# Kernel tuning notes

Measured on AMD Instinct MI355X. Metric: run time of the kernel, lower is better.

## Reference

```python
import jax, jax.numpy as jnp
import numpy as np

I4_CLIP = 7.0
NUM_HEADS = 16
NUM_KV_HEADS = 4
HEAD_DIM = 64
ROPE_BASE = 10000.0


def fake_quant_i4(w):
    # per-row int4 symmetric fake quantization with straight-through estimator
    row_max = jnp.maximum(jnp.max(jnp.abs(w), axis=-1, keepdims=True), 1e-8)
    scale = row_max / I4_CLIP
    w_deq = jnp.clip(jnp.round(w / scale), -I4_CLIP, I4_CLIP) * scale
    return w + jax.lax.stop_gradient(w_deq - w)


def rms_norm(x):
    eps = jnp.asarray(jnp.finfo(x.dtype).eps, x.dtype)
    return x * jax.lax.rsqrt(jnp.mean(x * x, axis=-1, keepdims=True) + eps)


def rope_cos_sin(seqlen, dtype):
    inv_freq = 1.0 / (ROPE_BASE ** (jnp.arange(0, HEAD_DIM, 2, dtype=jnp.float32) / HEAD_DIM))
    freqs = jnp.outer(jnp.arange(seqlen, dtype=jnp.float32), inv_freq)  # [S, hd/2]
    return jnp.cos(freqs).astype(dtype), jnp.sin(freqs).astype(dtype)


def apply_rotary(x, cos, sin):
    # x: [B, H, S, hd]; cos/sin: [S, hd/2] broadcast over B, H
    half = x.shape[-1] // 2
    x1, x2 = x[..., :half], x[..., half:]
    return jnp.concatenate((x1 * cos + x2 * sin, -x1 * sin + x2 * cos), axis=-1)


def setup_inputs() -> dict:
    key = jax.random.key(0)
    ks = jax.random.split(key, 6)
    dim = NUM_HEADS * HEAD_DIM
    kv_dim = NUM_KV_HEADS * HEAD_DIM
    return {
        "x": jax.random.normal(ks[0], (2, 2048, dim), jnp.float32),
        "w_q": jax.random.normal(ks[1], (dim, dim), jnp.float32) * 0.02,
        "w_k": jax.random.normal(ks[2], (kv_dim, dim), jnp.float32) * 0.02,
        "w_v": jax.random.normal(ks[3], (kv_dim, dim), jnp.float32) * 0.02,
        "w_proj": jax.random.normal(ks[4], (dim, dim), jnp.float32) * 0.02,
        "q_gain": jnp.ones((NUM_HEADS,), jnp.float32),
    }


def reference(x, w_q, w_k, w_v, w_proj, q_gain):
    bsz, seqlen, dim = x.shape
    rep = NUM_HEADS // NUM_KV_HEADS

    wq, wk, wv, wp = (fake_quant_i4(w) for w in (w_q, w_k, w_v, w_proj))

    # projections: F.linear(x, W) = x @ W.T -> [B, S, out]; split heads -> [B, H, S, hd]
    q = (x @ wq.T).reshape(bsz, seqlen, NUM_HEADS, HEAD_DIM).transpose(0, 2, 1, 3)
    k = (x @ wk.T).reshape(bsz, seqlen, NUM_KV_HEADS, HEAD_DIM).transpose(0, 2, 1, 3)
    v = (x @ wv.T).reshape(bsz, seqlen, NUM_KV_HEADS, HEAD_DIM).transpose(0, 2, 1, 3)

    q, k = rms_norm(q), rms_norm(k)
    cos, sin = rope_cos_sin(seqlen, q.dtype)
    q = apply_rotary(q, cos, sin)
    k = apply_rotary(k, cos, sin)
    q = q * q_gain.astype(q.dtype)[None, :, None, None]

    # GQA: expand kv heads
    k = jnp.repeat(k, rep, axis=1)
    v = jnp.repeat(v, rep, axis=1)

    # causal SDPA
    scale = 1.0 / np.sqrt(HEAD_DIM)
    scores = jnp.einsum("bhqd,bhkd->bhqk", q, k) * scale
    causal = jnp.tril(jnp.ones((seqlen, seqlen), dtype=bool))
    scores = jnp.where(causal, scores, jnp.asarray(-jnp.inf, scores.dtype))
    attn = jax.nn.softmax(scores, axis=-1)
    y = jnp.einsum("bhqk,bhkd->bhqd", attn, v)

    y = y.transpose(0, 2, 1, 3).reshape(bsz, seqlen, dim)
    return y @ wp.T
```

## Files before the change

kernel.cpp:

```cpp
#include <hip/hip_runtime.h>


typedef __bf16 bf16x8 __attribute__((ext_vector_type(8)));
typedef __bf16 bf16x4 __attribute__((ext_vector_type(4)));
typedef float  f32x4  __attribute__((ext_vector_type(4)));

__device__ __forceinline__ unsigned short f2bf(float f) {
  __bf16 h = (__bf16)f;
  return __builtin_bit_cast(unsigned short, h);
}

__global__ void prep(const float* __restrict__ wq, const float* __restrict__ wk,
                     const float* __restrict__ wv, const float* __restrict__ wp,
                     const float* __restrict__ x,
                     unsigned short* __restrict__ wqkv,
                     unsigned short* __restrict__ wpb,
                     unsigned short* __restrict__ x_bf) {
  int bid = blockIdx.x;
  int t = threadIdx.x;
  if (bid >= 2560) {
    int i = ((bid - 2560) * 256 + t) * 4;
    float4 f = *(const float4*)(x + i);
    ushort4 o;
    o.x = f2bf(f.x); o.y = f2bf(f.y); o.z = f2bf(f.z); o.w = f2bf(f.w);
    *(ushort4*)(x_bf + i) = o;
    return;
  }
  int row = bid;
  const float* s;
  unsigned short* d;
  if (row < 1024)      { s = wq + (size_t)row * 1024;          d = wqkv + (size_t)row * 1024; }
  else if (row < 1280) { s = wk + (size_t)(row - 1024) * 1024; d = wqkv + (size_t)row * 1024; }
  else if (row < 1536) { s = wv + (size_t)(row - 1280) * 1024; d = wqkv + (size_t)row * 1024; }
  else                 { s = wp + (size_t)(row - 1536) * 1024; d = wpb + (size_t)(row - 1536) * 1024; }
  float4 v = *(const float4*)(s + t * 4);
  float mx = fmaxf(fmaxf(fabsf(v.x), fabsf(v.y)), fmaxf(fabsf(v.z), fabsf(v.w)));
#pragma unroll
  for (int m = 1; m < 64; m <<= 1) mx = fmaxf(mx, __shfl_xor(mx, m));
  __shared__ float smx[4];
  if ((t & 63) == 0) smx[t >> 6] = mx;
  __syncthreads();
  mx = fmaxf(fmaxf(smx[0], smx[1]), fmaxf(smx[2], smx[3]));
  mx = fmaxf(mx, 1e-8f);
  float scale = mx / 7.0f;
  float q0 = fminf(fmaxf(rintf(v.x / scale), -7.0f), 7.0f);
  float q1 = fminf(fmaxf(rintf(v.y / scale), -7.0f), 7.0f);
  float q2 = fminf(fmaxf(rintf(v.z / scale), -7.0f), 7.0f);
  float q3 = fminf(fmaxf(rintf(v.w / scale), -7.0f), 7.0f);
  ushort4 o;
  o.x = f2bf(q0 * scale); o.y = f2bf(q1 * scale);
  o.z = f2bf(q2 * scale); o.w = f2bf(q3 * scale);
  *(ushort4*)(d + t * 4) = o;
}

#define GLDS(g, l)                                                            \
  __builtin_amdgcn_global_load_lds((const __attribute__((address_space(1))) void*)(g), \
                                   (__attribute__((address_space(3))) void*)(l), 16, 0, 0)

__global__ __launch_bounds__(512, 4) void gemm_bt(
    const unsigned short* __restrict__ A, const unsigned short* __restrict__ Bw,
    float* __restrict__ C, int N, int K, int nbn) {
  int bm = blockIdx.x / nbn, bn = blockIdx.x % nbn;
  int tid = threadIdx.x, w = tid >> 6, lane = tid & 63;
  int l15 = lane & 15, lh = lane >> 4;
  __shared__ __align__(16) unsigned short ldsA[2][128 * 64];
  __shared__ __align__(16) unsigned short ldsB[2][128 * 64];
  int wr = w >> 1, wc = w & 1;
  f32x4 zero = {0.f, 0.f, 0.f, 0.f};
  f32x4 acc[2][4];
#pragma unroll
  for (int i = 0; i < 2; i++)
#pragma unroll
    for (int j = 0; j < 4; j++) acc[i][j] = zero;

  int srow = lane >> 3, schunk = (lane & 7) ^ (lane >> 3);
  const unsigned short* gA0 = A  + (size_t)(bm * 128 + srow) * K + schunk * 8;
  const unsigned short* gB0 = Bw + (size_t)(bn * 128 + srow) * K + schunk * 8;

  int nk = K >> 6;
#pragma unroll
  for (int it = 0; it < 2; it++) {
    int seg = w * 2 + it;
    GLDS(gA0 + (size_t)(seg * 8) * K, (unsigned short*)ldsA[0] + seg * 512);
    GLDS(gB0 + (size_t)(seg * 8) * K, (unsigned short*)ldsB[0] + seg * 512);
  }
  __syncthreads();
  int cur = 0;
  for (int kt = 0; kt < nk; kt++) {
    if (kt + 1 < nk) {
      int k0 = (kt + 1) * 64;
#pragma unroll
      for (int it = 0; it < 2; it++) {
        int seg = w * 2 + it;
        GLDS(gA0 + (size_t)(seg * 8) * K + k0, (unsigned short*)ldsA[cur ^ 1] + seg * 512);
        GLDS(gB0 + (size_t)(seg * 8) * K + k0, (unsigned short*)ldsB[cur ^ 1] + seg * 512);
      }
    }
    const unsigned short* cA = ldsA[cur];
    const unsigned short* cB = ldsB[cur];
#pragma unroll
    for (int ks = 0; ks < 2; ks++) {
      bf16x8 af[2], bfr[4];
#pragma unroll
      for (int fm = 0; fm < 2; fm++) {
        int row = wr * 32 + fm * 16 + l15;
        int slot = (ks * 4 + lh) ^ (row & 7);
        af[fm] = *(const bf16x8*)(cA + row * 64 + slot * 8);
      }
#pragma unroll
      for (int fn = 0; fn < 4; fn++) {
        int row = wc * 64 + fn * 16 + l15;
        int slot = (ks * 4 + lh) ^ (row & 7);
        bfr[fn] = *(const bf16x8*)(cB + row * 64 + slot * 8);
      }
#pragma unroll
      for (int fm = 0; fm < 2; fm++)
#pragma unroll
        for (int fn = 0; fn < 4; fn++)
          acc[fm][fn] = __builtin_amdgcn_mfma_f32_16x16x32_bf16(af[fm], bfr[fn], acc[fm][fn], 0, 0, 0);
    }
    __syncthreads();
    cur ^= 1;
  }
#pragma unroll
  for (int fm = 0; fm < 2; fm++) {
    int r0 = bm * 128 + wr * 32 + fm * 16 + lh * 4;
#pragma unroll
    for (int fn = 0; fn < 4; fn++) {
      int c = bn * 128 + wc * 64 + fn * 16 + l15;
#pragma unroll
      for (int reg = 0; reg < 4; reg++)
        C[(size_t)(r0 + reg) * N + c] = acc[fm][fn][reg];
    }
  }
}

__global__ __launch_bounds__(512, 4) void gemm_qkv(
    const unsigned short* __restrict__ A, const unsigned short* __restrict__ Bw,
    const float* __restrict__ gainp,
    unsigned short* __restrict__ qb, unsigned short* __restrict__ kbp,
    unsigned short* __restrict__ vbp) {
  const int K = 1024;
  int bm = blockIdx.x / 12, bn = blockIdx.x % 12;
  int tid = threadIdx.x, w = tid >> 6, lane = tid & 63;
  int l15 = lane & 15, lh = lane >> 4;
  __shared__ __align__(16) unsigned short ldsA[2][128 * 64];
  __shared__ __align__(16) unsigned short ldsB[2][128 * 64];
  int wr = w >> 1, wc = w & 1;
  f32x4 zero = {0.f, 0.f, 0.f, 0.f};
  f32x4 acc[2][4];
#pragma unroll
  for (int i = 0; i < 2; i++)
#pragma unroll
    for (int j = 0; j < 4; j++) acc[i][j] = zero;

  int srow = lane >> 3, schunk = (lane & 7) ^ (lane >> 3);
  const unsigned short* gA0 = A  + (size_t)(bm * 128 + srow) * K + schunk * 8;
  const unsigned short* gB0 = Bw + (size_t)(bn * 128 + srow) * K + schunk * 8;

#pragma unroll
  for (int it = 0; it < 2; it++) {
    int seg = w * 2 + it;
    GLDS(gA0 + (size_t)(seg * 8) * K, (unsigned short*)ldsA[0] + seg * 512);
    GLDS(gB0 + (size_t)(seg * 8) * K, (unsigned short*)ldsB[0] + seg * 512);
  }
  __syncthreads();
  int cur = 0;
  for (int kt = 0; kt < 16; kt++) {
    if (kt + 1 < 16) {
      int k0 = (kt + 1) * 64;
#pragma unroll
      for (int it = 0; it < 2; it++) {
        int seg = w * 2 + it;
        GLDS(gA0 + (size_t)(seg * 8) * K + k0, (unsigned short*)ldsA[cur ^ 1] + seg * 512);
        GLDS(gB0 + (size_t)(seg * 8) * K + k0, (unsigned short*)ldsB[cur ^ 1] + seg * 512);
      }
    }
    const unsigned short* cA = ldsA[cur];
    const unsigned short* cB = ldsB[cur];
#pragma unroll
    for (int ks = 0; ks < 2; ks++) {
      bf16x8 af[2], bfr[4];
#pragma unroll
      for (int fm = 0; fm < 2; fm++) {
        int row = wr * 32 + fm * 16 + l15;
        int slot = (ks * 4 + lh) ^ (row & 7);
        af[fm] = *(const bf16x8*)(cA + row * 64 + slot * 8);
      }
#pragma unroll
      for (int fn = 0; fn < 4; fn++) {
        int row = wc * 64 + fn * 16 + l15;
        int slot = (ks * 4 + lh) ^ (row & 7);
        bfr[fn] = *(const bf16x8*)(cB + row * 64 + slot * 8);
      }
#pragma unroll
      for (int fm = 0; fm < 2; fm++)
#pragma unroll
        for (int fn = 0; fn < 4; fn++)
          acc[fm][fn] = __builtin_amdgcn_mfma_f32_16x16x32_bf16(af[fm], bfr[fn], acc[fm][fn], 0, 0, 0);
    }
    __syncthreads();
    cur ^= 1;
  }

  int hid = bn * 2 + wc;
  int rbase = bm * 128 + wr * 32;
  if (hid >= 20) {
    int vh = hid - 20;
#pragma unroll
    for (int fm = 0; fm < 2; fm++)
#pragma unroll
      for (int reg = 0; reg < 4; reg++) {
        int r = rbase + fm * 16 + lh * 4 + reg;
        int b = r >> 11, s = r & 2047;
        unsigned short* dst = vbp + (((size_t)(b * 4 + vh) * 2048 + s) << 6);
#pragma unroll
        for (int fn = 0; fn < 4; fn++)
          dst[fn * 16 + l15] = f2bf(acc[fm][fn][reg]);
      }
  } else {
    bool isq = hid < 16;
    float gn = isq ? gainp[hid] : 1.0f;
    float invf0 = __expf(-0.28782313662425572f * (float)l15);
    float invf1 = __expf(-0.28782313662425572f * (float)(l15 + 16));
#pragma unroll
    for (int fm = 0; fm < 2; fm++)
#pragma unroll
      for (int reg = 0; reg < 4; reg++) {
        float y0 = acc[fm][0][reg], y1 = acc[fm][1][reg];
        float y2 = acc[fm][2][reg], y3 = acc[fm][3][reg];
        float ss = y0 * y0 + y1 * y1 + y2 * y2 + y3 * y3;
        ss += __shfl_xor(ss, 1); ss += __shfl_xor(ss, 2);
        ss += __shfl_xor(ss, 4); ss += __shfl_xor(ss, 8);
        float rn = rsqrtf(ss * 0.015625f + 1.1920929e-7f);
        y0 *= rn; y1 *= rn; y2 *= rn; y3 *= rn;
        int r = rbase + fm * 16 + lh * 4 + reg;
        int b = r >> 11, s = r & 2047;
        float c0, s0n, c1, s1n;
        __sincosf((float)s * invf0, &s0n, &c0);
        __sincosf((float)s * invf1, &s1n, &c1);
        float o0 = (y0 * c0 + y2 * s0n) * gn;
        float o1 = (y1 * c1 + y3 * s1n) * gn;
        float o2 = (y2 * c0 - y0 * s0n) * gn;
        float o3 = (y3 * c1 - y1 * s1n) * gn;
        unsigned short* dst = isq
          ? qb  + (((size_t)(b * 16 + hid) * 2048 + s) << 6)
          : kbp + (((size_t)(b * 4 + (hid - 16)) * 2048 + s) << 6);
        dst[l15]      = f2bf(o0);
        dst[l15 + 16] = f2bf(o1);
        dst[l15 + 32] = f2bf(o2);
        dst[l15 + 48] = f2bf(o3);
      }
  }
}

__global__ void v_transpose(const unsigned short* __restrict__ vbp,
                            unsigned short* __restrict__ vt) {
  int bid = blockIdx.x;
  int st = bid & 31, bk = bid >> 5;
  __shared__ unsigned short tile[64][72];
  int t = threadIdx.x;
  int sl = t >> 2, d0 = (t & 3) * 16;
  const unsigned short* src = vbp + (((size_t)bk * 2048 + st * 64 + sl) << 6) + d0;
  *(ushort4*)&tile[sl][d0]      = *(const ushort4*)(src);
  *(ushort4*)&tile[sl][d0 + 4]  = *(const ushort4*)(src + 4);
  *(ushort4*)&tile[sl][d0 + 8]  = *(const ushort4*)(src + 8);
  *(ushort4*)&tile[sl][d0 + 12] = *(const ushort4*)(src + 12);
  __syncthreads();
  int d = t >> 2, p0 = (t & 3) * 16;
  unsigned short* dst = vt + ((size_t)bk * 64 + d) * 2048 + st * 64 + p0;
#pragma unroll
  for (int jo = 0; jo < 16; jo += 4) {
    ushort4 a;
#pragma unroll
    for (int j = 0; j < 4; j++) {
      int p = p0 + jo + j;
      int c = ((p & 3) << 4) | (p >> 2);
      ((unsigned short*)&a)[j] = tile[c][d];
    }
    *(ushort4*)(dst + jo) = a;
  }
}

#define PSTR 72

template<bool MASK>
__device__ __forceinline__ void attn_tile(
    int kv0, int q0, int l15, int lh, float M2,
    const unsigned short* ldsK, const unsigned short* ldsV, unsigned short* pw,
    const bf16x8 (&qf)[2][2], float (&lsum)[2][4], f32x4 (&o)[2][4]) {
  const float K2 = 0.18033688011112042f;
  f32x4 zero = {0.f, 0.f, 0.f, 0.f};
  f32x4 sc[2][4];
#pragma unroll
  for (int fm = 0; fm < 2; fm++)
#pragma unroll
    for (int fn = 0; fn < 4; fn++) sc[fm][fn] = zero;
#pragma unroll
  for (int ks = 0; ks < 2; ks++) {
    bf16x8 kf[4];
#pragma unroll
    for (int fn = 0; fn < 4; fn++) {
      int row = fn * 16 + l15;
      int slot = (ks * 4 + lh) ^ (row & 7);
      kf[fn] = *(const bf16x8*)(ldsK + row * 64 + slot * 8);
    }
#pragma unroll
    for (int fm = 0; fm < 2; fm++)
#pragma unroll
      for (int fn = 0; fn < 4; fn++)
        sc[fm][fn] = __builtin_amdgcn_mfma_f32_16x16x32_bf16(qf[fm][ks], kf[fn], sc[fm][fn], 0, 0, 0);
  }
  bf16x8 vf[2][4];
#pragma unroll
  for (int ks2 = 0; ks2 < 2; ks2++)
#pragma unroll
    for (int fn = 0; fn < 4; fn++) {
      int row = fn * 16 + l15;
      int slot = (ks2 * 4 + lh) ^ (row & 7);
      vf[ks2][fn] = *(const bf16x8*)(ldsV + row * 64 + slot * 8);
    }
#pragma unroll
  for (int fm = 0; fm < 2; fm++)
#pragma unroll
    for (int r = 0; r < 4; r++) {
      bf16x4 pk;
      float ls = 0.f;
#pragma unroll
      for (int fn = 0; fn < 4; fn++) {
        float s = __builtin_fmaf(sc[fm][fn][r], K2, -M2);
        if (MASK) {
          int col = kv0 + fn * 16 + l15;
          int row = q0 + fm * 16 + lh * 4 + r;
          if (col > row) s = -1e30f;
        }
        float p = __builtin_amdgcn_exp2f(s);
        ls += p;
        pk[fn] = (__bf16)p;
      }
      *(bf16x4*)(pw + (fm * 16 + lh * 4 + r) * PSTR + l15 * 4) = pk;
      lsum[fm][r] += ls;
    }
  asm volatile("s_waitcnt lgkmcnt(0)" ::: "memory");
  __builtin_amdgcn_sched_barrier(0);
#pragma unroll
  for (int ks2 = 0; ks2 < 2; ks2++) {
    bf16x8 pf[2];
#pragma unroll
    for (int fm = 0; fm < 2; fm++)
      pf[fm] = *(const bf16x8*)(pw + (fm * 16 + l15) * PSTR + ks2 * 32 + lh * 8);
#pragma unroll
    for (int fm = 0; fm < 2; fm++)
#pragma unroll
      for (int fn = 0; fn < 4; fn++)
        o[fm][fn] = __builtin_amdgcn_mfma_f32_16x16x32_bf16(pf[fm], vf[ks2][fn], o[fm][fn], 0, 0, 0);
  }
}

__global__ __launch_bounds__(256, 3) void attn_fwd(
    const unsigned short* __restrict__ qbuf, const unsigned short* __restrict__ kb,
    const unsigned short* __restrict__ vtb, const float* __restrict__ gain,
    unsigned short* __restrict__ ob, unsigned short* __restrict__ pO,
    float* __restrict__ pL) {
  int bid = blockIdx.x;
  int cid = bid >> 5;
  int bh = bid & 31;
  int b = bh >> 4, h = bh & 15;
  int qb = 0, cum = 0;
  for (int q = 0; q < 16; q++) {
    int ncq = (2 * q + 5) >> 2;
    if (cid < cum + ncq) { qb = q; break; }
    cum += ncq;
  }
  int nt = 2 * qb + 2;
  int nc = (2 * qb + 5) >> 2;
  int ch = cid - cum;
  int base = nt / nc, rem = nt % nc;
  int t0 = ch * base + (ch < rem ? ch : rem);
  int t1 = t0 + base + (ch < rem ? 1 : 0);
  bool direct = (nc == 1);

  int tid = threadIdx.x;
  int w = tid >> 6, lane = tid & 63;
  int l15 = lane & 15, lh = lane >> 4;
  int q0 = qb * 128 + w * 32;
  int kvh = h >> 2;
  const unsigned short* Q  = qbuf + (size_t)(b * 16 + h) * (2048 * 64);
  const unsigned short* Kg = kb   + (size_t)(b * 4 + kvh) * (2048 * 64);
  const unsigned short* Vg = vtb  + (size_t)(b * 4 + kvh) * (64 * 2048);

  __shared__ __align__(16) unsigned short ldsK[2][64 * 64];
  __shared__ __align__(16) unsigned short ldsV[2][64 * 64];
  __shared__ __align__(16) unsigned short plds[4][32 * PSTR];
  unsigned short* pw = plds[w];

  float gn = gain[h];
  float M2 = __builtin_fmaf(fabsf(gn), 1.46f, 0.02f);

  bf16x8 qf[2][2];
#pragma unroll
  for (int fm = 0; fm < 2; fm++)
#pragma unroll
    for (int ks = 0; ks < 2; ks++)
      qf[fm][ks] = *(const bf16x8*)(Q + (q0 + fm * 16 + l15) * 64 + ks * 32 + lh * 8);

  f32x4 zero = {0.f, 0.f, 0.f, 0.f};
  f32x4 o[2][4];
  float lsum[2][4];
#pragma unroll
  for (int fm = 0; fm < 2; fm++)
#pragma unroll
    for (int r = 0; r < 4; r++) { lsum[fm][r] = 0.f; o[fm][r] = zero; }

  int srow = lane >> 3;
  int schunk = (lane & 7) ^ (lane >> 3);
  int full = q0 >> 6;

#pragma unroll
  for (int it = 0; it < 2; it++) {
    int seg = w * 2 + it;
    GLDS(Kg + (size_t)(t0 * 64 + seg * 8 + srow) * 64 + schunk * 8,
         (unsigned short*)ldsK[0] + seg * 512);
    GLDS(Vg + (size_t)(seg * 8 + srow) * 2048 + t0 * 64 + schunk * 8,
         (unsigned short*)ldsV[0] + seg * 512);
  }
  __syncthreads();
  int cur = 0;
  for (int t = t0; t < t1; t++) {
    int kv0 = t * 64;
    if (t + 1 < t1) {
      int kn = kv0 + 64;
#pragma unroll
      for (int it = 0; it < 2; it++) {
        int seg = w * 2 + it;
        GLDS(Kg + (size_t)(kn + seg * 8 + srow) * 64 + schunk * 8,
             (unsigned short*)ldsK[cur ^ 1] + seg * 512);
        GLDS(Vg + (size_t)(seg * 8 + srow) * 2048 + kn + schunk * 8,
             (unsigned short*)ldsV[cur ^ 1] + seg * 512);
      }
    }
    if (t < full)
      attn_tile<false>(kv0, q0, l15, lh, M2, ldsK[cur], ldsV[cur], pw, qf, lsum, o);
    else if (kv0 <= q0 + 31)
      attn_tile<true>(kv0, q0, l15, lh, M2, ldsK[cur], ldsV[cur], pw, qf, lsum, o);
    __syncthreads();
    cur ^= 1;
  }

  if (direct) {
#pragma unroll
    for (int fm = 0; fm < 2; fm++)
#pragma unroll
      for (int r = 0; r < 4; r++) {
        float l = lsum[fm][r];
        l += __shfl_xor(l, 1); l += __shfl_xor(l, 2);
        l += __shfl_xor(l, 4); l += __shfl_xor(l, 8);
        float inv = 1.0f / l;
        int row = q0 + fm * 16 + lh * 4 + r;
#pragma unroll
        for (int fn = 0; fn < 4; fn++)
          ob[(size_t)(b * 2048 + row) * 1024 + h * 64 + fn * 16 + l15] =
              f2bf(o[fm][fn][r] * inv);
      }
  } else {
    int slot = bh * 70 + (cid - 2);
    unsigned short* po = pO + ((size_t)slot << 13);
    float* pl = pL + slot * 128;
#pragma unroll
    for (int fm = 0; fm < 2; fm++)
#pragma unroll
      for (int r = 0; r < 4; r++) {
        float l = lsum[fm][r];
        l += __shfl_xor(l, 1); l += __shfl_xor(l, 2);
        l += __shfl_xor(l, 4); l += __shfl_xor(l, 8);
        int row = w * 32 + fm * 16 + lh * 4 + r;
        if (l15 == 0) pl[row] = l;
        bf16x4 pv;
#pragma unroll
        for (int fn = 0; fn < 4; fn++) pv[fn] = (__bf16)o[fm][fn][r];
        *(bf16x4*)(po + row * 64 + l15 * 4) = pv;
      }
  }
}

__global__ __launch_bounds__(128) void attn_finalize(
    const unsigned short* __restrict__ pO, const float* __restrict__ pL,
    unsigned short* __restrict__ ob) {
  int bid = blockIdx.x;
  int qb = 2 + bid % 14;
  int bh = bid / 14;
  int b = bh >> 4, h = bh & 15;
  int cum = 0;
  for (int q = 0; q < 16; q++) {
    if (q == qb) break;
    cum += (2 * q + 5) >> 2;
  }
  int nc = (2 * qb + 5) >> 2;
  int s0 = bh * 70 + (cum - 2);

  int row = threadIdx.x;
  float acc[64];
#pragma unroll
  for (int j = 0; j < 64; j++) acc[j] = 0.f;
  float l = 0.f;
  for (int c = 0; c < nc; c++) {
    const unsigned short* po = pO + (((size_t)(s0 + c)) << 13) + row * 64;
    l += pL[(s0 + c) * 128 + row];
#pragma unroll
    for (int j = 0; j < 8; j++) {
      uint4 u = *(const uint4*)(po + j * 8);
      const unsigned short* us = (const unsigned short*)&u;
#pragma unroll
      for (int e = 0; e < 8; e++) {
        unsigned int bits = (unsigned int)us[e] << 16;
        acc[j * 8 + e] += __builtin_bit_cast(float, bits);
      }
    }
  }
  float inv = 1.0f / l;
  unsigned short* dst = ob + (size_t)(b * 2048 + qb * 128 + row) * 1024 + h * 64;
  unsigned short outv[64];
#pragma unroll
  for (int c = 0; c < 64; c++) {
    int pos = (c & 15) * 4 + (c >> 4);
    outv[c] = f2bf(acc[pos] * inv);
  }
#pragma unroll
  for (int j = 0; j < 8; j++)
    *(uint4*)(dst + j * 8) = *(const uint4*)(outv + j * 8);
}

extern "C" void kernel_launch(void* const* d_in, const int* in_sizes, int n_in,
                              void* d_out, int out_size, void* d_ws, size_t ws_size,
                              hipStream_t stream) {
  const float* x    = (const float*)d_in[0];
  const float* w_q  = (const float*)d_in[1];
  const float* w_k  = (const float*)d_in[2];
  const float* w_v  = (const float*)d_in[3];
  const float* w_p  = (const float*)d_in[4];
  const float* gain = (const float*)d_in[5];
  float* out = (float*)d_out;

  char* ws = (char*)d_ws;
  unsigned short* x_bf  = (unsigned short*)ws;
  unsigned short* wqkv  = (unsigned short*)(ws + (8u << 20));
  unsigned short* wp    = (unsigned short*)(ws + (11u << 20));
  unsigned short* qbuf  = (unsigned short*)(ws + (13u << 20));
  unsigned short* kbuf  = (unsigned short*)(ws + (21u << 20));
  unsigned short* vbuf  = (unsigned short*)(ws + (23u << 20));
  unsigned short* vtbuf = (unsigned short*)(ws + (25u << 20));
  unsigned short* aout  = (unsigned short*)(ws + (27u << 20));
  unsigned short* pO    = (unsigned short*)(ws + (35u << 20));
  float*          pL    = (float*)(ws + (73u << 20));

  prep<<<6656, 256, 0, stream>>>(w_q, w_k, w_v, w_p, x, wqkv, wp, x_bf);
  gemm_qkv<<<32 * 12, 512, 0, stream>>>(x_bf, wqkv, gain, qbuf, kbuf, vbuf);
  v_transpose<<<256, 256, 0, stream>>>(vbuf, vtbuf);
  attn_fwd<<<2304, 256, 0, stream>>>(qbuf, kbuf, vtbuf, gain, aout, pO, pL);
  attn_finalize<<<448, 128, 0, stream>>>(pO, pL, aout);
  gemm_bt<<<32 * 8, 512, 0, stream>>>(aout, wp, out, 1024, 1024, 8);
}
```

Measured before the change: 102.1 us.

## Switch attention to 32x32x16 MFMA with register-resident P via permlane swap

New measurement: 100.0 us. 1.02x faster.

```diff
diff --git a/kernel.cpp b/kernel.cpp
--- a/kernel.cpp
+++ b/kernel.cpp
@@ -2,8 +2,9 @@
 
 
 typedef __bf16 bf16x8 __attribute__((ext_vector_type(8)));
-typedef __bf16 bf16x4 __attribute__((ext_vector_type(4)));
 typedef float  f32x4  __attribute__((ext_vector_type(4)));
+typedef float  f32x16 __attribute__((ext_vector_type(16)));
+typedef int    i32x4  __attribute__((ext_vector_type(4)));
 
 __device__ __forceinline__ unsigned short f2bf(float f) {
   __bf16 h = (__bf16)f;
@@ -273,87 +274,72 @@
   for (int jo = 0; jo < 16; jo += 4) {
     ushort4 a;
 #pragma unroll
-    for (int j = 0; j < 4; j++) {
-      int p = p0 + jo + j;
-      int c = ((p & 3) << 4) | (p >> 2);
-      ((unsigned short*)&a)[j] = tile[c][d];
-    }
+    for (int j = 0; j < 4; j++)
+      ((unsigned short*)&a)[j] = tile[p0 + jo + j][d];
     *(ushort4*)(dst + jo) = a;
   }
 }
-
-#define PSTR 72
 
 template<bool MASK>
 __device__ __forceinline__ void attn_tile(
-    int kv0, int q0, int l15, int lh, float M2,
-    const unsigned short* ldsK, const unsigned short* ldsV, unsigned short* pw,
-    const bf16x8 (&qf)[2][2], float (&lsum)[2][4], f32x4 (&o)[2][4]) {
+    int kv0, int q0, int l31, int hi, float M2,
+    const unsigned short* ldsK, const unsigned short* ldsV,
+    const bf16x8 (&qf)[4], float& lsum, f32x16 (&o)[2]) {
   const float K2 = 0.18033688011112042f;
-  f32x4 zero = {0.f, 0.f, 0.f, 0.f};
-  f32x4 sc[2][4];
-#pragma unroll
-  for (int fm = 0; fm < 2; fm++)
-#pragma unroll
-    for (int fn = 0; fn < 4; fn++) sc[fm][fn] = zero;
-#pragma unroll
-  for (int ks = 0; ks < 2; ks++) {
-    bf16x8 kf[4];
-#pragma unroll
-    for (int fn = 0; fn < 4; fn++) {
-      int row = fn * 16 + l15;
-      int slot = (ks * 4 + lh) ^ (row & 7);
-      kf[fn] = *(const bf16x8*)(ldsK + row * 64 + slot * 8);
-    }
-#pragma unroll
-    for (int fm = 0; fm < 2; fm++)
-#pragma unroll
-      for (int fn = 0; fn < 4; fn++)
-        sc[fm][fn] = __builtin_amdgcn_mfma_f32_16x16x32_bf16(qf[fm][ks], kf[fn], sc[fm][fn], 0, 0, 0);
-  }
-  bf16x8 vf[2][4];
-#pragma unroll
-  for (int ks2 = 0; ks2 < 2; ks2++)
-#pragma unroll
-    for (int fn = 0; fn < 4; fn++) {
-      int row = fn * 16 + l15;
-      int slot = (ks2 * 4 + lh) ^ (row & 7);
-      vf[ks2][fn] = *(const bf16x8*)(ldsV + row * 64 + slot * 8);
-    }
-#pragma unroll
-  for (int fm = 0; fm < 2; fm++)
-#pragma unroll
-    for (int r = 0; r < 4; r++) {
-      bf16x4 pk;
-      float ls = 0.f;
-#pragma unroll
-      for (int fn = 0; fn < 4; fn++) {
-        float s = __builtin_fmaf(sc[fm][fn][r], K2, -M2);
+  f32x16 sc[2];
+#pragma unroll
+  for (int i = 0; i < 16; i++) { sc[0][i] = 0.f; sc[1][i] = 0.f; }
+#pragma unroll
+  for (int ks = 0; ks < 4; ks++) {
+    int slot0 = (2 * ks + hi) ^ (l31 & 7);
+    bf16x8 kf0 = *(const bf16x8*)(ldsK + l31 * 64 + slot0 * 8);
+    int row1 = 32 + l31;
+    int slot1 = (2 * ks + hi) ^ (row1 & 7);
+    bf16x8 kf1 = *(const bf16x8*)(ldsK + row1 * 64 + slot1 * 8);
+    sc[0] = __builtin_amdgcn_mfma_f32_32x32x16_bf16(kf0, qf[ks], sc[0], 0, 0, 0);
+    sc[1] = __builtin_amdgcn_mfma_f32_32x32x16_bf16(kf1, qf[ks], sc[1], 0, 0, 0);
+  }
+  unsigned int Wp[2][4][2];
+  float ls = 0.f;
+  int rowq = q0 + l31;
+#pragma unroll
+  for (int fn = 0; fn < 2; fn++)
+#pragma unroll
+    for (int g = 0; g < 4; g++) {
+      float p4[4];
+#pragma unroll
+      for (int m = 0; m < 4; m++) {
+        int r = 4 * g + m;
+        float s = __builtin_fmaf(sc[fn][r], K2, -M2);
         if (MASK) {
-          int col = kv0 + fn * 16 + l15;
-          int row = q0 + fm * 16 + lh * 4 + r;
-          if (col > row) s = -1e30f;
+          int col = kv0 + fn * 32 + m + 8 * g + 4 * hi;
+          if (col > rowq) s = -1e30f;
         }
         float p = __builtin_amdgcn_exp2f(s);
         ls += p;
-        pk[fn] = (__bf16)p;
-      }
-      *(bf16x4*)(pw + (fm * 16 + lh * 4 + r) * PSTR + l15 * 4) = pk;
-      lsum[fm][r] += ls;
-    }
-  asm volatile("s_waitcnt lgkmcnt(0)" ::: "memory");
-  __builtin_amdgcn_sched_barrier(0);
-#pragma unroll
-  for (int ks2 = 0; ks2 < 2; ks2++) {
-    bf16x8 pf[2];
-#pragma unroll
-    for (int fm = 0; fm < 2; fm++)
-      pf[fm] = *(const bf16x8*)(pw + (fm * 16 + l15) * PSTR + ks2 * 32 + lh * 8);
-#pragma unroll
-    for (int fm = 0; fm < 2; fm++)
-#pragma unroll
-      for (int fn = 0; fn < 4; fn++)
-        o[fm][fn] = __builtin_amdgcn_mfma_f32_16x16x32_bf16(pf[fm], vf[ks2][fn], o[fm][fn], 0, 0, 0);
+        p4[m] = p;
+      }
+      asm("v_cvt_pk_bf16_f32 %0, %1, %2" : "=v"(Wp[fn][g][0]) : "v"(p4[0]), "v"(p4[1]));
+      asm("v_cvt_pk_bf16_f32 %0, %1, %2" : "=v"(Wp[fn][g][1]) : "v"(p4[2]), "v"(p4[3]));
+    }
+  lsum += ls;
+#pragma unroll
+  for (int ksg = 0; ksg < 4; ksg++) {
+    int fn = ksg >> 1, e = ksg & 1;
+    unsigned int u0 = Wp[fn][2 * e][0], u1 = Wp[fn][2 * e + 1][0];
+    unsigned int u2 = Wp[fn][2 * e][1], u3 = Wp[fn][2 * e + 1][1];
+    asm("v_permlane32_swap_b32 %0, %1" : "+v"(u0), "+v"(u1));
+    asm("v_permlane32_swap_b32 %0, %1" : "+v"(u2), "+v"(u3));
+    i32x4 pw;
+    pw[0] = (int)u0; pw[1] = (int)u2; pw[2] = (int)u1; pw[3] = (int)u3;
+    bf16x8 pf = __builtin_bit_cast(bf16x8, pw);
+    int slot0 = (2 * ksg + hi) ^ (l31 & 7);
+    bf16x8 v0 = *(const bf16x8*)(ldsV + l31 * 64 + slot0 * 8);
+    int row1 = 32 + l31;
+    int slot1 = (2 * ksg + hi) ^ (row1 & 7);
+    bf16x8 v1 = *(const bf16x8*)(ldsV + row1 * 64 + slot1 * 8);
+    o[0] = __builtin_amdgcn_mfma_f32_32x32x16_bf16(pf, v0, o[0], 0, 0, 0);
+    o[1] = __builtin_amdgcn_mfma_f32_32x32x16_bf16(pf, v1, o[1], 0, 0, 0);
   }
 }
 
@@ -382,7 +368,7 @@
 
   int tid = threadIdx.x;
   int w = tid >> 6, lane = tid & 63;
-  int l15 = lane & 15, lh = lane >> 4;
+  int l31 = lane & 31, hi = lane >> 5;
   int q0 = qb * 128 + w * 32;
   int kvh = h >> 2;
   const unsigned short* Q  = qbuf + (size_t)(b * 16 + h) * (2048 * 64);
@@ -391,26 +377,19 @@
 
   __shared__ __align__(16) unsigned short ldsK[2][64 * 64];
   __shared__ __align__(16) unsigned short ldsV[2][64 * 64];
-  __shared__ __align__(16) unsigned short plds[4][32 * PSTR];
-  unsigned short* pw = plds[w];
 
   float gn = gain[h];
   float M2 = __builtin_fmaf(fabsf(gn), 1.46f, 0.02f);
 
-  bf16x8 qf[2][2];
-#pragma unroll
-  for (int fm = 0; fm < 2; fm++)
-#pragma unroll
-    for (int ks = 0; ks < 2; ks++)
-      qf[fm][ks] = *(const bf16x8*)(Q + (q0 + fm * 16 + l15) * 64 + ks * 32 + lh * 8);
-
-  f32x4 zero = {0.f, 0.f, 0.f, 0.f};
-  f32x4 o[2][4];
-  float lsum[2][4];
-#pragma unroll
-  for (int fm = 0; fm < 2; fm++)
-#pragma unroll
-    for (int r = 0; r < 4; r++) { lsum[fm][r] = 0.f; o[fm][r] = zero; }
+  bf16x8 qf[4];
+#pragma unroll
+  for (int ks = 0; ks < 4; ks++)
+    qf[ks] = *(const bf16x8*)(Q + (size_t)(q0 + l31) * 64 + ks * 16 + hi * 8);
+
+  f32x16 o[2];
+#pragma unroll
+  for (int i = 0; i < 16; i++) { o[0][i] = 0.f; o[1][i] = 0.f; }
+  float lsum = 0.f;
 
   int srow = lane >> 3;
   int schunk = (lane & 7) ^ (lane >> 3);
@@ -440,46 +419,36 @@
       }
     }
     if (t < full)
-      attn_tile<false>(kv0, q0, l15, lh, M2, ldsK[cur], ldsV[cur], pw, qf, lsum, o);
+      attn_tile<false>(kv0, q0, l31, hi, M2, ldsK[cur], ldsV[cur], qf, lsum, o);
     else if (kv0 <= q0 + 31)
-      attn_tile<true>(kv0, q0, l15, lh, M2, ldsK[cur], ldsV[cur], pw, qf, lsum, o);
+      attn_tile<true>(kv0, q0, l31, hi, M2, ldsK[cur], ldsV[cur], qf, lsum, o);
     __syncthreads();
     cur ^= 1;
   }
 
+  float lred = lsum + __shfl_xor(lsum, 32);
   if (direct) {
-#pragma unroll
-    for (int fm = 0; fm < 2; fm++)
-#pragma unroll
-      for (int r = 0; r < 4; r++) {
-        float l = lsum[fm][r];
-        l += __shfl_xor(l, 1); l += __shfl_xor(l, 2);
-        l += __shfl_xor(l, 4); l += __shfl_xor(l, 8);
-        float inv = 1.0f / l;
-        int row = q0 + fm * 16 + lh * 4 + r;
-#pragma unroll
-        for (int fn = 0; fn < 4; fn++)
-          ob[(size_t)(b * 2048 + row) * 1024 + h * 64 + fn * 16 + l15] =
-              f2bf(o[fm][fn][r] * inv);
-      }
+    float linv = 1.0f / lred;
+#pragma unroll
+    for (int r = 0; r < 16; r++) {
+      int qr = (r & 3) + 8 * (r >> 2) + 4 * hi;
+      float iv = __shfl(linv, qr);
+      size_t rb = (size_t)(b * 2048 + q0 + qr) * 1024 + h * 64;
+      ob[rb + l31]      = f2bf(o[0][r] * iv);
+      ob[rb + 32 + l31] = f2bf(o[1][r] * iv);
+    }
   } else {
     int slot = bh * 70 + (cid - 2);
     unsigned short* po = pO + ((size_t)slot << 13);
     float* pl = pL + slot * 128;
-#pragma unroll
-    for (int fm = 0; fm < 2; fm++)
-#pragma unroll
-      for (int r = 0; r < 4; r++) {
-        float l = lsum[fm][r];
-        l += __shfl_xor(l, 1); l += __shfl_xor(l, 2);
-        l += __shfl_xor(l, 4); l += __shfl_xor(l, 8);
-        int row = w * 32 + fm * 16 + lh * 4 + r;
-        if (l15 == 0) pl[row] = l;
-        bf16x4 pv;
-#pragma unroll
-        for (int fn = 0; fn < 4; fn++) pv[fn] = (__bf16)o[fm][fn][r];
-        *(bf16x4*)(po + row * 64 + l15 * 4) = pv;
-      }
+    if (lane < 32) pl[w * 32 + l31] = lred;
+#pragma unroll
+    for (int r = 0; r < 16; r++) {
+      int qr = (r & 3) + 8 * (r >> 2) + 4 * hi;
+      int row = w * 32 + qr;
+      po[row * 64 + l31]      = f2bf(o[0][r]);
+      po[row * 64 + 32 + l31] = f2bf(o[1][r]);
+    }
   }
 }
 
@@ -521,10 +490,7 @@
   unsigned short* dst = ob + (size_t)(b * 2048 + qb * 128 + row) * 1024 + h * 64;
   unsigned short outv[64];
 #pragma unroll
-  for (int c = 0; c < 64; c++) {
-    int pos = (c & 15) * 4 + (c >> 4);
-    outv[c] = f2bf(acc[pos] * inv);
-  }
+  for (int c = 0; c < 64; c++) outv[c] = f2bf(acc[c] * inv);
 #pragma unroll
   for (int j = 0; j < 8; j++)
     *(uint4*)(dst + j * 8) = *(const uint4*)(outv + j * 8);
```
